# Performance work log

Hardware: AMD Instinct MI355X
Metric: run time of the kernel (lower is better)

Reference implementation:

```python
import jax, jax.numpy as jnp
import numpy as np

NUM_CLASSES = 20
MEM_SIZE = 512      # memory_bank_size
MAX_VIEWS = 512
TEMP = 0.1
MOMENTUM = 0.999
IGNORE_IDX = 255
AUX_IDX = 254
EPS = 1e-12


def _nearest_resize(gt, Ho, Wo):
    # torch F.interpolate(mode='nearest'): src = floor(dst * in/out)
    B, Hi, Wi = gt.shape
    ri = (jnp.arange(Ho) * Hi) // Ho
    ci = (jnp.arange(Wo) * Wi) // Wo
    return gt[:, ri][:, :, ci]


def _norm_flat(p):
    # L2-normalize over channels, then [B, C, H, W] -> [B, H*W, C]
    p = p / jnp.maximum(jnp.linalg.norm(p, axis=1, keepdims=True), EPS)
    B, C = p.shape[0], p.shape[1]
    return p.reshape(B, C, -1).transpose(0, 2, 1)


def setup_inputs() -> dict:
    key = jax.random.key(0)
    k1, k2, k3, k4, k5 = jax.random.split(key, 5)
    B, D, H, W = 4, 256, 128, 128
    Hg, Wg = 512, 512
    return {
        'main_proj': jax.random.normal(k1, (B, D, H, W), dtype=jnp.float32),
        'main_gt': jax.random.randint(k2, (B, Hg, Wg), 0, NUM_CLASSES).astype(jnp.int64),
        'aux_proj': jax.random.normal(k3, (B, D, H, W), dtype=jnp.float32),
        'aux_gt': jax.random.randint(k4, (B, Hg, Wg), 0, NUM_CLASSES).astype(jnp.int64),
        'memory_bank': jax.random.normal(k5, (NUM_CLASSES, MEM_SIZE, D), dtype=jnp.float32),
    }


def reference(main_proj, main_gt, aux_proj, aux_gt, memory_bank):
    C, M, D = memory_bank.shape
    B, _, H, W = main_proj.shape
    mg = _nearest_resize(main_gt, H, W)
    ag = _nearest_resize(aux_gt, aux_proj.shape[2], aux_proj.shape[3])

    embd = jnp.concatenate([_norm_flat(main_proj), _norm_flat(aux_proj)], axis=1)
    embd = embd.reshape(-1, D)                       # [N, D]
    label = jnp.concatenate([mg.reshape(B, -1), ag.reshape(B, -1)], axis=1).reshape(-1)

    valid = label != IGNORE_IDX
    label = jnp.where(label == AUX_IDX, C - 1, label)

    # per-class gather: stable argsort puts class-c pixels first (deterministic
    # stand-in for torch.randperm selection)
    masks = (label[None, :] == jnp.arange(C)[:, None]) & valid[None, :]   # [C, N]
    counts = masks.sum(axis=1)                                           # [C]
    order = jnp.argsort(~masks, axis=1, stable=True)[:, :M]              # [C, M]
    sel = embd[order]                                                    # [C, M, D]
    sel_valid = jnp.arange(M)[None, :] < counts[:, None]                 # [C, M]

    # momentum scatter-update to memory bank (no grad through features)
    upd = MOMENTUM * memory_bank + (1.0 - MOMENTUM) * jax.lax.stop_gradient(sel)
    upd = upd / jnp.maximum(jnp.linalg.norm(upd, axis=2, keepdims=True), EPS)
    bank = jnp.where(sel_valid[..., None], upd, memory_bank)             # [C, M, D]

    # anchors from current batch (with grad)
    V = min(MAX_VIEWS, M)
    anchors = sel[:, :V].reshape(C * V, D)
    a_valid = sel_valid[:, :V].reshape(-1)
    a_lbl = jnp.repeat(jnp.arange(C), V)

    # contrastive samples from updated bank (constant w.r.t. grad)
    contras = bank.reshape(C * M, D)
    c_valid = jnp.linalg.norm(bank, axis=2).reshape(-1) > 0
    c_lbl = jnp.repeat(jnp.arange(C), M)

    # InfoNCE with masked softmax over valid contrastive columns
    scores = (anchors @ contras.T) / TEMP                                # [A, K]
    scores = jnp.where(c_valid[None, :], scores, -1e9)
    logp = jax.nn.log_softmax(scores, axis=1)
    pos = ((a_lbl[:, None] == c_lbl[None, :]) & c_valid[None, :]).astype(scores.dtype)
    pos_sum = (pos * logp).sum(axis=1)
    pos_cnt = pos.sum(axis=1)
    va = (pos_cnt > 0) & a_valid
    mlpp = jnp.where(va, pos_sum / jnp.maximum(pos_cnt, 1.0), 0.0)
    loss = -mlpp.sum() / jnp.maximum(va.sum(), 1).astype(scores.dtype)
    return loss
```

## Files before the change

kernel.cpp:

```cpp
#include <hip/hip_runtime.h>
#include <cstdint>
#include <math.h>

#define NCLS  20
#define MSZ   512
#define DIM   256
#define HW    16384
#define NPIX  131072
#define AROWS 10240
#define TEMP_INV 10.0f
#define EXP2K 14.4269504088896f

typedef __attribute__((ext_vector_type(8))) short bf16x8;
typedef __attribute__((ext_vector_type(4))) float f32x4;

__device__ __forceinline__ short f2bf(float f) {
    unsigned u = __float_as_uint(f);
    unsigned r = (u + 0x7FFFu + ((u >> 16) & 1u)) >> 16;
    return (short)r;
}
__device__ __forceinline__ float bf2f(short s) {
    return __uint_as_float(((unsigned)(unsigned short)s) << 16);
}
__device__ __forceinline__ float fexp2(float x) {
    float r;
    asm volatile("v_exp_f32 %0, %1" : "=v"(r) : "v"(x));
    return r;
}
__device__ __forceinline__ void gld16(const void* g, void* l) {
    __builtin_amdgcn_global_load_lds(
        (const __attribute__((address_space(1))) unsigned int*)(uintptr_t)g,
        (__attribute__((address_space(3))) unsigned int*)(unsigned int)(uintptr_t)l,
        16, 0, 0);
}

#define ZREG_FLOATS 15488

__global__ __launch_bounds__(256) void k_hist(const int* __restrict__ mg,
                                              const int* __restrict__ ag,
                                              int* __restrict__ labels,
                                              int* __restrict__ hist,
                                              int* __restrict__ pix2row,
                                              float* __restrict__ zreg) {
    int chunk = blockIdx.x, t = threadIdx.x;
    int lane = t & 63;
    int gi = chunk * 256 + t;
    if (gi < ZREG_FLOATS) zreg[gi] = 0.0f;

    int n = gi;
    int b = n >> 15, r = n & 32767;
    const int* g = (r < HW) ? mg : ag;
    int p = (r < HW) ? r : (r - HW);
    int h = p >> 7, w = p & 127;
    int lab = g[(((size_t)b * 512) + (size_t)(h << 2)) * 512 + (size_t)(w << 2)];
    if (lab == 255) lab = -1;
    else if (lab == 254) lab = NCLS - 1;
    labels[n] = lab;
    pix2row[n] = -1;

    __shared__ int cnt20[NCLS];
    if (t < NCLS) cnt20[t] = 0;
    __syncthreads();
#pragma unroll
    for (int c = 0; c < NCLS; ++c) {
        unsigned long long m = __ballot(lab == c);
        if (lane == 0 && m) atomicAdd(&cnt20[c], __popcll(m));
    }
    __syncthreads();
    if (t < NCLS) hist[t * 512 + chunk] = cnt20[t];
}

__global__ __launch_bounds__(256) void k_write(const int* __restrict__ labels,
                                               const int* __restrict__ hist,
                                               int* __restrict__ pix2row,
                                               int* __restrict__ counts) {
    int chunk = blockIdx.x, t = threadIdx.x;
    int lane = t & 63, wv = t >> 6;
    __shared__ int cbase[NCLS];
    __shared__ int wcnt2[4][NCLS];

#pragma unroll
    for (int cc = 0; cc < 5; ++cc) {
        int c = wv * 5 + cc;
        int s = 0;
        for (int j = lane; j < chunk; j += 64) s += hist[c * 512 + j];
#pragma unroll
        for (int o = 32; o > 0; o >>= 1) s += __shfl_down(s, o, 64);
        if (lane == 0) cbase[c] = s;
    }

    int n = chunk * 256 + t;
    int lab = labels[n];
    int myrank = 0;
#pragma unroll
    for (int c = 0; c < NCLS; ++c) {
        unsigned long long m = __ballot(lab == c);
        if (lane == 0) wcnt2[wv][c] = __popcll(m);
        if (lab == c) myrank = __popcll(m & ((1ull << lane) - 1ull));
    }
    __syncthreads();
    if (lab >= 0) {
        int base = cbase[lab] + myrank;
        for (int w = 0; w < wv; ++w) base += wcnt2[w][lab];
        if (base < MSZ) pix2row[n] = lab * MSZ + base;
    }
    if (chunk == 511 && t < NCLS)
        counts[t] = cbase[t] + wcnt2[0][t] + wcnt2[1][t] + wcnt2[2][t] + wcnt2[3][t];
}

__global__ __launch_bounds__(256) void k_scatter(const float* __restrict__ mainp,
                                                 const float* __restrict__ auxp,
                                                 const int* __restrict__ pix2row,
                                                 float* __restrict__ xF) {
    int idx = blockIdx.x * 256 + threadIdx.x;
    int p4 = idx & 4095;
    int ch = (idx >> 12) & 255;
    int bs = idx >> 20;
    int b = bs >> 1, src = bs & 1;
    int4 pr = *(const int4*)(pix2row + bs * HW + p4 * 4);
    if ((pr.x & pr.y & pr.z & pr.w) < 0) return;
    const float* base = (src ? auxp : mainp) + (size_t)b * DIM * HW + (size_t)ch * HW;
    float4 v = *(const float4*)(base + p4 * 4);
    if (pr.x >= 0) xF[(size_t)pr.x * DIM + ch] = v.x;
    if (pr.y >= 0) xF[(size_t)pr.y * DIM + ch] = v.y;
    if (pr.z >= 0) xF[(size_t)pr.z * DIM + ch] = v.z;
    if (pr.w >= 0) xF[(size_t)pr.w * DIM + ch] = v.w;
}

__global__ __launch_bounds__(256) void k_nbc(const float* __restrict__ xF,
                                             const float* __restrict__ bank,
                                             const int* __restrict__ counts,
                                             short* __restrict__ anchorsB,
                                             short* __restrict__ contrasB,
                                             int* __restrict__ c_valid,
                                             float* __restrict__ S,
                                             int* __restrict__ pcnt) {
    int blk = blockIdx.x;
    int c = blk >> 5;
    int t = threadIdx.x, lane = t & 63, wv = t >> 6;
    int cc = counts[c];
    int base = blk * 16;
    float sacc[4] = {0.f, 0.f, 0.f, 0.f};
    int vcnt = 0;

    for (int it = 0; it < 4; ++it) {
        int a = base + it * 4 + wv;
        int m = a & 511;
        float4 xv = *(const float4*)&xF[(size_t)a * DIM + lane * 4];
        float x[4] = {xv.x, xv.y, xv.z, xv.w};
        float ss = x[0]*x[0] + x[1]*x[1] + x[2]*x[2] + x[3]*x[3];
#pragma unroll
        for (int o = 1; o < 64; o <<= 1) ss += __shfl_xor(ss, o, 64);
        float scale = 1.0f / fmaxf(sqrtf(ss), 1e-12f);
        float ax[4];
#pragma unroll
        for (int q = 0; q < 4; ++q) ax[q] = x[q] * scale;
        short4 oa;
        oa.x = f2bf(ax[0]); oa.y = f2bf(ax[1]); oa.z = f2bf(ax[2]); oa.w = f2bf(ax[3]);
        *(short4*)&anchorsB[(size_t)a * DIM + lane * 4] = oa;

        bool upd = m < cc;
        float4 bv = *(const float4*)&bank[(size_t)a * DIM + lane * 4];
        float u[4];
        u[0] = upd ? 0.999f * bv.x + 0.001f * ax[0] : bv.x;
        u[1] = upd ? 0.999f * bv.y + 0.001f * ax[1] : bv.y;
        u[2] = upd ? 0.999f * bv.z + 0.001f * ax[2] : bv.z;
        u[3] = upd ? 0.999f * bv.w + 0.001f * ax[3] : bv.w;
        float ss2 = u[0]*u[0] + u[1]*u[1] + u[2]*u[2] + u[3]*u[3];
#pragma unroll
        for (int o = 1; o < 64; o <<= 1) ss2 += __shfl_xor(ss2, o, 64);
        float nrm = sqrtf(ss2);
        float inv = 1.0f / fmaxf(nrm, 1e-12f);
        short oc[4];
        oc[0] = f2bf(upd ? u[0] * inv : bv.x);
        oc[1] = f2bf(upd ? u[1] * inv : bv.y);
        oc[2] = f2bf(upd ? u[2] * inv : bv.z);
        oc[3] = f2bf(upd ? u[3] * inv : bv.w);
        *(short4*)&contrasB[(size_t)a * DIM + lane * 4] = *(short4*)oc;
        bool valid = nrm > 0.0f;
        if (lane == 0) {
            c_valid[a] = valid ? 1 : 0;
            vcnt += valid ? 1 : 0;
        }
        if (valid) {
#pragma unroll
            for (int q = 0; q < 4; ++q) sacc[q] += bf2f(oc[q]);
        }
    }

    __shared__ float s4[4][DIM];
    __shared__ int pv[4];
#pragma unroll
    for (int q = 0; q < 4; ++q) s4[wv][lane * 4 + q] = sacc[q];
    if (lane == 0) pv[wv] = vcnt;
    __syncthreads();
    float s = s4[0][t] + s4[1][t] + s4[2][t] + s4[3][t];
    atomicAdd(&S[c * DIM + t], s);
    if (t == 0) atomicAdd(&pcnt[c], pv[0] + pv[1] + pv[2] + pv[3]);
}

__global__ __launch_bounds__(512, 4) void k_score(const short* __restrict__ A,
                                                  const short* __restrict__ Bc,
                                                  const int* __restrict__ c_valid,
                                                  float* __restrict__ row_sumexp) {
    __shared__ short As[128 * 64];
    __shared__ short Bs[256 * 64];
    const int t = threadIdx.x;
    const int lane = t & 63, wv = t >> 6;
    const int wr = wv & 1, wc = wv >> 1;
    const int qr = lane >> 4, qc = lane & 15;
    const int s7 = qc & 7;
    const int row0 = blockIdx.x * 128, col0 = blockIdx.y * 256;

    const int rl8 = t >> 3;
    const int sdat = (t & 7) ^ (rl8 & 7);
    const short* Ag = A  + (size_t)row0 * DIM;
    const short* Bg = Bc + (size_t)col0 * DIM;

    const int sl0 = ((0 + qr) ^ s7) * 8;
    const int sl1 = ((4 + qr) ^ s7) * 8;

    f32x4 acc[4][4] = {};

    auto stage = [&](int kt) {
#pragma unroll
        for (int r = 0; r < 2; ++r)
            gld16(Ag + (size_t)(r * 64 + rl8) * DIM + kt * 64 + sdat * 8,
                  &As[(r * 64 + wv * 8) * 64]);
#pragma unroll
        for (int r = 0; r < 4; ++r)
            gld16(Bg + (size_t)(r * 64 + rl8) * DIM + kt * 64 + sdat * 8,
                  &Bs[(r * 64 + wv * 8) * 64]);
    };

    stage(0);
    for (int kt = 0; kt < 4; ++kt) {
        asm volatile("s_waitcnt vmcnt(0)" ::: "memory");
        asm volatile("s_barrier" ::: "memory");

        bf16x8 a0[4], b0[4], a1[4], b1[4];
#pragma unroll
        for (int rt = 0; rt < 4; ++rt)
            a0[rt] = *(const bf16x8*)&As[(wr * 64 + rt * 16 + qc) * 64 + sl0];
#pragma unroll
        for (int ct = 0; ct < 4; ++ct)
            b0[ct] = *(const bf16x8*)&Bs[(wc * 64 + ct * 16 + qc) * 64 + sl0];
#pragma unroll
        for (int rt = 0; rt < 4; ++rt)
#pragma unroll
            for (int ct = 0; ct < 4; ++ct)
                acc[rt][ct] = __builtin_amdgcn_mfma_f32_16x16x32_bf16(a0[rt], b0[ct], acc[rt][ct], 0, 0, 0);
#pragma unroll
        for (int rt = 0; rt < 4; ++rt)
            a1[rt] = *(const bf16x8*)&As[(wr * 64 + rt * 16 + qc) * 64 + sl1];
#pragma unroll
        for (int ct = 0; ct < 4; ++ct)
            b1[ct] = *(const bf16x8*)&Bs[(wc * 64 + ct * 16 + qc) * 64 + sl1];

        asm volatile("s_waitcnt lgkmcnt(0)" ::: "memory");
        __builtin_amdgcn_sched_barrier(0);
        asm volatile("s_barrier" ::: "memory");
        if (kt < 3) stage(kt + 1);

#pragma unroll
        for (int rt = 0; rt < 4; ++rt)
#pragma unroll
            for (int ct = 0; ct < 4; ++ct)
                acc[rt][ct] = __builtin_amdgcn_mfma_f32_16x16x32_bf16(a1[rt], b1[ct], acc[rt][ct], 0, 0, 0);
    }

    float cm[4];
#pragma unroll
    for (int ct = 0; ct < 4; ++ct)
        cm[ct] = c_valid[col0 + wc * 64 + ct * 16 + qc] ? 1.0f : 0.0f;
#pragma unroll
    for (int rt = 0; rt < 4; ++rt)
#pragma unroll
        for (int r = 0; r < 4; ++r) {
            float e = cm[0] * fexp2(acc[rt][0][r] * EXP2K)
                    + cm[1] * fexp2(acc[rt][1][r] * EXP2K)
                    + cm[2] * fexp2(acc[rt][2][r] * EXP2K)
                    + cm[3] * fexp2(acc[rt][3][r] * EXP2K);
#pragma unroll
            for (int o = 1; o < 16; o <<= 1) e += __shfl_xor(e, o, 64);
            if (qc == 0)
                atomicAdd(&row_sumexp[row0 + wr * 64 + rt * 16 + qr * 4 + r], e);
        }
}

__global__ __launch_bounds__(256) void k_fin(const short* __restrict__ anchorsB,
                                             const float* __restrict__ S,
                                             const int* __restrict__ counts,
                                             const int* __restrict__ pcnt,
                                             const float* __restrict__ row_sumexp,
                                             float* __restrict__ facc,
                                             int* __restrict__ done_cnt,
                                             float* __restrict__ out) {
    int blk = blockIdx.x;
    int c = blk >> 5;
    int t = threadIdx.x, lane = t & 63, wv = t >> 6;
    int pc = pcnt[c], cc = counts[c];
    float lsum = 0.0f, vc = 0.0f;

    for (int it = 0; it < 4; ++it) {
        int a = blk * 16 + it * 4 + wv;
        short4 a4 = *(const short4*)&anchorsB[(size_t)a * DIM + lane * 4];
        float4 s4 = *(const float4*)&S[c * DIM + lane * 4];
        float dot = bf2f(a4.x) * s4.x + bf2f(a4.y) * s4.y
                  + bf2f(a4.z) * s4.z + bf2f(a4.w) * s4.w;
#pragma unroll
        for (int o = 1; o < 64; o <<= 1) dot += __shfl_xor(dot, o, 64);
        if (lane == 0 && (a & 511) < cc && pc > 0) {
            float lse = logf(row_sumexp[a]);
            lsum += (TEMP_INV * dot - (float)pc * lse) / (float)pc;
            vc += 1.0f;
        }
    }

    __shared__ float wls[4], wvc[4];
    if (lane == 0) { wls[wv] = lsum; wvc[wv] = vc; }
    __syncthreads();
    if (t == 0) {
        atomicAdd(&facc[0], wls[0] + wls[1] + wls[2] + wls[3]);
        atomicAdd(&facc[1], wvc[0] + wvc[1] + wvc[2] + wvc[3]);
        __threadfence();
        unsigned d = atomicAdd((unsigned*)done_cnt, 1u);
        if (d == 639u) {
            __threadfence();
            float L = atomicAdd(&facc[0], 0.0f);
            float V = atomicAdd(&facc[1], 0.0f);
            out[0] = -L / fmaxf(V, 1.0f);
        }
    }
}

extern "C" void kernel_launch(void* const* d_in, const int* in_sizes, int n_in,
                              void* d_out, int out_size, void* d_ws, size_t ws_size,
                              hipStream_t stream) {
    const float* main_proj = (const float*)d_in[0];
    const int*   main_gt   = (const int*)d_in[1];
    const float* aux_proj  = (const float*)d_in[2];
    const int*   aux_gt    = (const int*)d_in[3];
    const float* bank      = (const float*)d_in[4];
    float* out = (float*)d_out;

    char* ws = (char*)d_ws;
    int*   labels     = (int*)ws;
    int*   hist       = (int*)(ws + 524288);
    int*   pix2row    = (int*)(ws + 565248);
    int*   c_valid    = (int*)(ws + 1089536);
    float* zreg       = (float*)(ws + 1130496);
    float* row_sumexp = zreg;
    float* S          = zreg + 10240;
    int*   pcnt       = (int*)(zreg + 15360);
    float* facc       = zreg + 15380;
    int*   done_cnt   = (int*)(zreg + 15382);
    int*   counts     = (int*)(ws + 1192448);
    float* xF         = (float*)(ws + 1192704);
    short* anchorsB   = (short*)(ws + 11678464);
    short* contrasB   = (short*)(ws + 16921344);

    k_hist<<<512, 256, 0, stream>>>(main_gt, aux_gt, labels, hist, pix2row, zreg);
    k_write<<<512, 256, 0, stream>>>(labels, hist, pix2row, counts);
    k_scatter<<<32768, 256, 0, stream>>>(main_proj, aux_proj, pix2row, xF);
    k_nbc<<<AROWS / 16, 256, 0, stream>>>(xF, bank, counts, anchorsB, contrasB,
                                          c_valid, S, pcnt);
    dim3 grid(AROWS / 128, AROWS / 256);
    k_score<<<grid, 512, 0, stream>>>(anchorsB, contrasB, c_valid, row_sumexp);
    k_fin<<<AROWS / 16, 256, 0, stream>>>(anchorsB, S, counts, pcnt, row_sumexp,
                                          facc, done_cnt, out);
}
```

Measured before the change: 276.2 us.

## Replace pixel-to-row scatter with row-to-pixel gather inside normalize kernel

```diff
diff --git a/kernel.cpp b/kernel.cpp
--- a/kernel.cpp
+++ b/kernel.cpp
@@ -40,12 +40,13 @@
                                               const int* __restrict__ ag,
                                               int* __restrict__ labels,
                                               int* __restrict__ hist,
-                                              int* __restrict__ pix2row,
+                                              int* __restrict__ row2pix,
                                               float* __restrict__ zreg) {
     int chunk = blockIdx.x, t = threadIdx.x;
     int lane = t & 63;
     int gi = chunk * 256 + t;
     if (gi < ZREG_FLOATS) zreg[gi] = 0.0f;
+    if (gi < AROWS) row2pix[gi] = -1;
 
     int n = gi;
     int b = n >> 15, r = n & 32767;
@@ -56,7 +57,6 @@
     if (lab == 255) lab = -1;
     else if (lab == 254) lab = NCLS - 1;
     labels[n] = lab;
-    pix2row[n] = -1;
 
     __shared__ int cnt20[NCLS];
     if (t < NCLS) cnt20[t] = 0;
@@ -72,7 +72,7 @@
 
 __global__ __launch_bounds__(256) void k_write(const int* __restrict__ labels,
                                                const int* __restrict__ hist,
-                                               int* __restrict__ pix2row,
+                                               int* __restrict__ row2pix,
                                                int* __restrict__ counts) {
     int chunk = blockIdx.x, t = threadIdx.x;
     int lane = t & 63, wv = t >> 6;
@@ -102,32 +102,15 @@
     if (lab >= 0) {
         int base = cbase[lab] + myrank;
         for (int w = 0; w < wv; ++w) base += wcnt2[w][lab];
-        if (base < MSZ) pix2row[n] = lab * MSZ + base;
+        if (base < MSZ) row2pix[lab * MSZ + base] = n;
     }
     if (chunk == 511 && t < NCLS)
         counts[t] = cbase[t] + wcnt2[0][t] + wcnt2[1][t] + wcnt2[2][t] + wcnt2[3][t];
 }
 
-__global__ __launch_bounds__(256) void k_scatter(const float* __restrict__ mainp,
-                                                 const float* __restrict__ auxp,
-                                                 const int* __restrict__ pix2row,
-                                                 float* __restrict__ xF) {
-    int idx = blockIdx.x * 256 + threadIdx.x;
-    int p4 = idx & 4095;
-    int ch = (idx >> 12) & 255;
-    int bs = idx >> 20;
-    int b = bs >> 1, src = bs & 1;
-    int4 pr = *(const int4*)(pix2row + bs * HW + p4 * 4);
-    if ((pr.x & pr.y & pr.z & pr.w) < 0) return;
-    const float* base = (src ? auxp : mainp) + (size_t)b * DIM * HW + (size_t)ch * HW;
-    float4 v = *(const float4*)(base + p4 * 4);
-    if (pr.x >= 0) xF[(size_t)pr.x * DIM + ch] = v.x;
-    if (pr.y >= 0) xF[(size_t)pr.y * DIM + ch] = v.y;
-    if (pr.z >= 0) xF[(size_t)pr.z * DIM + ch] = v.z;
-    if (pr.w >= 0) xF[(size_t)pr.w * DIM + ch] = v.w;
-}
-
-__global__ __launch_bounds__(256) void k_nbc(const float* __restrict__ xF,
+__global__ __launch_bounds__(256) void k_nbc(const float* __restrict__ mainp,
+                                             const float* __restrict__ auxp,
+                                             const int* __restrict__ row2pix,
                                              const float* __restrict__ bank,
                                              const int* __restrict__ counts,
                                              short* __restrict__ anchorsB,
@@ -143,11 +126,23 @@
     float sacc[4] = {0.f, 0.f, 0.f, 0.f};
     int vcnt = 0;
 
+#pragma unroll
     for (int it = 0; it < 4; ++it) {
         int a = base + it * 4 + wv;
         int m = a & 511;
-        float4 xv = *(const float4*)&xF[(size_t)a * DIM + lane * 4];
-        float x[4] = {xv.x, xv.y, xv.z, xv.w};
+        int n = row2pix[a];
+        float x[4];
+        if (n >= 0) {
+            int b = n >> 15, r = n & 32767;
+            const float* src = (r < HW) ? mainp : auxp;
+            int p = (r < HW) ? r : (r - HW);
+            const float* gp = src + (size_t)b * DIM * HW + p;
+#pragma unroll
+            for (int q = 0; q < 4; ++q)
+                x[q] = gp[(size_t)(lane * 4 + q) * HW];
+        } else {
+            x[0] = x[1] = x[2] = x[3] = 0.0f;
+        }
         float ss = x[0]*x[0] + x[1]*x[1] + x[2]*x[2] + x[3]*x[3];
 #pragma unroll
         for (int o = 1; o < 64; o <<= 1) ss += __shfl_xor(ss, o, 64);
@@ -347,7 +342,7 @@
     char* ws = (char*)d_ws;
     int*   labels     = (int*)ws;
     int*   hist       = (int*)(ws + 524288);
-    int*   pix2row    = (int*)(ws + 565248);
+    int*   row2pix    = (int*)(ws + 565248);
     int*   c_valid    = (int*)(ws + 1089536);
     float* zreg       = (float*)(ws + 1130496);
     float* row_sumexp = zreg;
@@ -356,15 +351,13 @@
     float* facc       = zreg + 15380;
     int*   done_cnt   = (int*)(zreg + 15382);
     int*   counts     = (int*)(ws + 1192448);
-    float* xF         = (float*)(ws + 1192704);
     short* anchorsB   = (short*)(ws + 11678464);
     short* contrasB   = (short*)(ws + 16921344);
 
-    k_hist<<<512, 256, 0, stream>>>(main_gt, aux_gt, labels, hist, pix2row, zreg);
-    k_write<<<512, 256, 0, stream>>>(labels, hist, pix2row, counts);
-    k_scatter<<<32768, 256, 0, stream>>>(main_proj, aux_proj, pix2row, xF);
-    k_nbc<<<AROWS / 16, 256, 0, stream>>>(xF, bank, counts, anchorsB, contrasB,
-                                          c_valid, S, pcnt);
+    k_hist<<<512, 256, 0, stream>>>(main_gt, aux_gt, labels, hist, row2pix, zreg);
+    k_write<<<512, 256, 0, stream>>>(labels, hist, row2pix, counts);
+    k_nbc<<<AROWS / 16, 256, 0, stream>>>(main_proj, aux_proj, row2pix, bank, counts,
+                                          anchorsB, contrasB, c_valid, S, pcnt);
     dim3 grid(AROWS / 128, AROWS / 256);
     k_score<<<grid, 512, 0, stream>>>(anchorsB, contrasB, c_valid, row_sumexp);
     k_fin<<<AROWS / 16, 256, 0, stream>>>(anchorsB, S, counts, pcnt, row_sumexp,
```

After: 260.1 us. 5.8% less time.
